# Optimization experiments

Measured on AMD Instinct MI355X. Metric: run time of the kernel, lower is better.

Reference implementation:

```python
import jax, jax.numpy as jnp
import numpy as np

D_MODEL = 768
NHEAD = 12
HEAD_DIM = D_MODEL // NHEAD


def setup_inputs() -> dict:
    key = jax.random.key(0)
    ks = jax.random.split(key, 7)
    s = 1.0 / np.sqrt(D_MODEL)
    x = jax.random.normal(ks[0], (8, 1024, D_MODEL), dtype=jnp.float32)
    Wq = jax.random.uniform(ks[1], (D_MODEL, D_MODEL), jnp.float32, -s, s)
    bq = jax.random.uniform(ks[2], (D_MODEL,), jnp.float32, -s, s)
    Wk = jax.random.uniform(ks[3], (D_MODEL, D_MODEL), jnp.float32, -s, s)
    bk = jax.random.uniform(ks[4], (D_MODEL,), jnp.float32, -s, s)
    Wv = jax.random.uniform(ks[5], (D_MODEL, D_MODEL), jnp.float32, -s, s)
    bv = jax.random.uniform(ks[6], (D_MODEL,), jnp.float32, -s, s)
    return {"x": x, "Wq": Wq, "bq": bq, "Wk": Wk, "bk": bk, "Wv": Wv, "bv": bv}


def reference(x, Wq, bq, Wk, bk, Wv, bv):
    B, S, D = x.shape
    # linear projections (torch Linear: x @ W.T + b)
    q = x @ Wq.T + bq
    k = x @ Wk.T + bk
    v = x @ Wv.T + bv
    # split heads: [B, S, H, Dh] -> [B, H, S, Dh]
    split = lambda t: t.reshape(B, S, NHEAD, HEAD_DIM).transpose(0, 2, 1, 3)
    q, k, v = split(q), split(k), split(v)
    scale = 1.0 / np.sqrt(HEAD_DIM)
    scores = jnp.einsum("bhqd,bhkd->bhqk", q, k) * scale  # [B,H,S,S]
    scores = jax.nn.softmax(scores, axis=-1)  # dropout p=0.0 -> identity
    h = jnp.einsum("bhqk,bhkd->bhqd", scores, v)  # [B,H,S,Dh]
    h = h.transpose(0, 2, 1, 3).reshape(B, S, D)
    return (h, scores)
```

## Files before the change

### kernel.cpp

```cpp
#include <hip/hip_runtime.h>

#define D_MODEL  768
#define NHEAD    12
#define HEAD_DIM 64
#define SEQ      1024
#define BATCH    8
#define NTOK     8192

typedef unsigned short u16;
typedef unsigned int   u32;
typedef float  f32x4  __attribute__((ext_vector_type(4)));
typedef __bf16 bf16x8 __attribute__((ext_vector_type(8)));

#define MFMA(a, b, c) __builtin_amdgcn_mfma_f32_16x16x32_bf16((a), (b), (c), 0, 0, 0)

__device__ __forceinline__ u16 f2bf(float f) {
    u32 u = __float_as_uint(f);
    u += 0x7fffu + ((u >> 16) & 1u);
    return (u16)(u >> 16);
}
__device__ __forceinline__ u32 pack2(float a, float b) {
    return (u32)f2bf(a) | ((u32)f2bf(b) << 16);
}
__device__ __forceinline__ bf16x8 ldfrag(const u16* p) {
    union { uint4 u; bf16x8 b; } c;
    c.u = *(const uint4*)p;
    return c.b;
}
__device__ __forceinline__ bf16x8 u2b(uint4 u) {
    union { uint4 u; bf16x8 b; } c;
    c.u = u;
    return c.b;
}
__device__ __forceinline__ float bflo(u32 u) { return __uint_as_float(u << 16); }
__device__ __forceinline__ float bfhi(u32 u) { return __uint_as_float(u & 0xffff0000u); }

__global__ __launch_bounds__(256)
void qkv_gemm(const float* __restrict__ x,
              const float* __restrict__ Wq, const float* __restrict__ bq,
              const float* __restrict__ Wk, const float* __restrict__ bk,
              const float* __restrict__ Wv, const float* __restrict__ bv,
              u16* __restrict__ qo, u16* __restrict__ ko, u16* __restrict__ vto)
{
    const int m0 = blockIdx.x * 64;
    const int n0 = blockIdx.y * 64;
    const int z  = blockIdx.z;
    const float* W    = (z == 0) ? Wq : (z == 1) ? Wk : Wv;
    const float* bias = (z == 0) ? bq : (z == 1) ? bk : bv;

    __shared__ u16 As[64][72];
    __shared__ u16 Bs[64][72];

    const int t    = threadIdx.x;
    const int lane = t & 63, wave = t >> 6;
    const int grp  = lane >> 4, l16 = lane & 15;
    const int wm   = (wave >> 1) * 32;
    const int wn   = (wave & 1) * 32;
    const int sr   = t >> 2;
    const int sc   = (t & 3) * 16;

    f32x4 acc[2][2] = {};

    for (int kt = 0; kt < D_MODEL; kt += 64) {
        const float* xp = x + (size_t)(m0 + sr) * D_MODEL + kt + sc;
        const float* wp = W + (size_t)(n0 + sr) * D_MODEL + kt + sc;
        const float4 x0 = ((const float4*)xp)[0], x1 = ((const float4*)xp)[1];
        const float4 x2 = ((const float4*)xp)[2], x3 = ((const float4*)xp)[3];
        const float4 w0 = ((const float4*)wp)[0], w1 = ((const float4*)wp)[1];
        const float4 w2 = ((const float4*)wp)[2], w3 = ((const float4*)wp)[3];
        __syncthreads();
        uint4 ua, ub;
        ua.x = pack2(x0.x, x0.y); ua.y = pack2(x0.z, x0.w);
        ua.z = pack2(x1.x, x1.y); ua.w = pack2(x1.z, x1.w);
        ub.x = pack2(x2.x, x2.y); ub.y = pack2(x2.z, x2.w);
        ub.z = pack2(x3.x, x3.y); ub.w = pack2(x3.z, x3.w);
        *(uint4*)&As[sr][sc]     = ua;
        *(uint4*)&As[sr][sc + 8] = ub;
        ua.x = pack2(w0.x, w0.y); ua.y = pack2(w0.z, w0.w);
        ua.z = pack2(w1.x, w1.y); ua.w = pack2(w1.z, w1.w);
        ub.x = pack2(w2.x, w2.y); ub.y = pack2(w2.z, w2.w);
        ub.z = pack2(w3.x, w3.y); ub.w = pack2(w3.z, w3.w);
        *(uint4*)&Bs[sr][sc]     = ua;
        *(uint4*)&Bs[sr][sc + 8] = ub;
        __syncthreads();
#pragma unroll
        for (int ks = 0; ks < 64; ks += 32) {
            const bf16x8 a0 = ldfrag(&As[wm + l16][ks + grp * 8]);
            const bf16x8 a1 = ldfrag(&As[wm + 16 + l16][ks + grp * 8]);
            const bf16x8 b0 = ldfrag(&Bs[wn + l16][ks + grp * 8]);
            const bf16x8 b1 = ldfrag(&Bs[wn + 16 + l16][ks + grp * 8]);
            acc[0][0] = MFMA(a0, b0, acc[0][0]);
            acc[0][1] = MFMA(a0, b1, acc[0][1]);
            acc[1][0] = MFMA(a1, b0, acc[1][0]);
            acc[1][1] = MFMA(a1, b1, acc[1][1]);
        }
    }

    u16* qk_out = (z == 0) ? qo : ko;
#pragma unroll
    for (int tn = 0; tn < 2; ++tn) {
        const int col = n0 + wn + tn * 16 + l16;
        const float bcol = bias[col];
#pragma unroll
        for (int tm = 0; tm < 2; ++tm) {
#pragma unroll
            for (int r = 0; r < 4; ++r) {
                const int row = m0 + wm + tm * 16 + grp * 4 + r;
                const u16 hv = f2bf(acc[tm][tn][r] + bcol);
                if (z < 2) {
                    qk_out[(size_t)row * D_MODEL + col] = hv;
                } else {
                    const int hh = col >> 6, dd = col & 63;
                    const int bb = row >> 10, ss = row & 1023;
                    vto[(((size_t)(bb * NHEAD + hh)) * HEAD_DIM + dd) * SEQ + ss] = hv;
                }
            }
        }
    }
}

__global__ __launch_bounds__(256, 2)
void attn_mfma(const u16* __restrict__ qb, const u16* __restrict__ kb,
               const u16* __restrict__ vtb, float* __restrict__ hout,
               float* __restrict__ sout)
{
    const int qt = blockIdx.x, h = blockIdx.y, b = blockIdx.z;
    const int t    = threadIdx.x;
    const int lane = t & 63, wave = t >> 6;
    const int grp  = lane >> 4, l16 = lane & 15;

    __shared__ u16 Qs[64][72];
    __shared__ u16 Ks[64][72];
    __shared__ u16 Vts[64][72];
    __shared__ u16 Ps[4][16][40];

    const size_t tok0 = (size_t)b * SEQ + qt * 64;
    const int    hb   = h * HEAD_DIM;
    const int    lr   = t >> 3, c0 = (t & 7) * 8;

    {
        const u16* qp = qb + (tok0 + lr) * D_MODEL + hb + c0;
        const uint4 v0 = *(const uint4*)qp;
        const uint4 v1 = *(const uint4*)(qp + (size_t)32 * D_MODEL);
        *(uint4*)&Qs[lr][c0]      = v0;
        *(uint4*)&Qs[lr + 32][c0] = v1;
    }
    __syncthreads();
    const bf16x8 qa0 = ldfrag(&Qs[wave * 16 + l16][grp * 8]);
    const bf16x8 qa1 = ldfrag(&Qs[wave * 16 + l16][32 + grp * 8]);

    const float scale = 0.125f;
    float ssum[4] = {0.f, 0.f, 0.f, 0.f};
    f32x4 accO[4] = {};
    uint4 preg[32];

    const u16* kbase = kb + (size_t)b * SEQ * D_MODEL + hb;
    const u16* vbase = vtb + ((size_t)(b * NHEAD + h) * HEAD_DIM + lr) * SEQ;

#pragma unroll
    for (int kt = 0; kt < 16; ++kt) {
        __syncthreads();
        {
            const u16* kp = kbase + (size_t)(kt * 64 + lr) * D_MODEL + c0;
            const uint4 v0 = *(const uint4*)kp;
            const uint4 v1 = *(const uint4*)(kp + (size_t)32 * D_MODEL);
            const u16* vp = vbase + kt * 64 + c0;
            const uint4 u0 = *(const uint4*)vp;
            const uint4 u1 = *(const uint4*)(vp + (size_t)32 * SEQ);
            *(uint4*)&Ks[lr][c0]       = v0;
            *(uint4*)&Ks[lr + 32][c0]  = v1;
            *(uint4*)&Vts[lr][c0]      = u0;
            *(uint4*)&Vts[lr + 32][c0] = u1;
        }
        __syncthreads();
#pragma unroll
        for (int half = 0; half < 2; ++half) {
#pragma unroll
            for (int sub = 0; sub < 2; ++sub) {
                const int ti = half * 2 + sub;
                const bf16x8 kb0 = ldfrag(&Ks[ti * 16 + l16][grp * 8]);
                const bf16x8 kb1 = ldfrag(&Ks[ti * 16 + l16][32 + grp * 8]);
                f32x4 c = {0.f, 0.f, 0.f, 0.f};
                c = MFMA(qa0, kb0, c);
                c = MFMA(qa1, kb1, c);
#pragma unroll
                for (int r = 0; r < 4; ++r) {
                    const float p = __expf(c[r] * scale);
                    ssum[r] += p;
                    Ps[wave][grp * 4 + r][sub * 16 + l16] = f2bf(p);
                }
            }
            const uint4 pw = *(const uint4*)&Ps[wave][l16][grp * 8];
            preg[kt * 2 + half] = pw;
            const bf16x8 pa = u2b(pw);
#pragma unroll
            for (int c4 = 0; c4 < 4; ++c4) {
                const bf16x8 vb = ldfrag(&Vts[c4 * 16 + l16][half * 32 + grp * 8]);
                accO[c4] = MFMA(pa, vb, accO[c4]);
            }
        }
    }

#pragma unroll
    for (int off = 1; off < 16; off <<= 1)
#pragma unroll
        for (int r = 0; r < 4; ++r) ssum[r] += __shfl_xor(ssum[r], off);
    float sinv[4];
#pragma unroll
    for (int r = 0; r < 4; ++r) sinv[r] = 1.0f / ssum[r];

    const int src = (l16 >> 2) * 16 + l16;
    const float t0 = __shfl(ssum[0], src), t1 = __shfl(ssum[1], src);
    const float t2 = __shfl(ssum[2], src), t3 = __shfl(ssum[3], src);
    const float sa = (l16 & 1) ? t1 : t0;
    const float sb = (l16 & 1) ? t3 : t2;
    const float sinvrow = 1.0f / ((l16 & 2) ? sb : sa);

#pragma unroll
    for (int c4 = 0; c4 < 4; ++c4)
#pragma unroll
        for (int r = 0; r < 4; ++r)
            hout[(tok0 + wave * 16 + grp * 4 + r) * D_MODEL + hb + c4 * 16 + l16] =
                accO[c4][r] * sinv[r];

    float* sp = sout + (size_t)(b * NHEAD + h) * SEQ * SEQ
              + (size_t)(qt * 64 + wave * 16 + l16) * SEQ + grp * 8;
#pragma unroll
    for (int kt = 0; kt < 16; ++kt) {
#pragma unroll
        for (int half = 0; half < 2; ++half) {
            const uint4 pw = preg[kt * 2 + half];
            float4 o0, o1;
            o0.x = bflo(pw.x) * sinvrow; o0.y = bfhi(pw.x) * sinvrow;
            o0.z = bflo(pw.y) * sinvrow; o0.w = bfhi(pw.y) * sinvrow;
            o1.x = bflo(pw.z) * sinvrow; o1.y = bfhi(pw.z) * sinvrow;
            o1.z = bflo(pw.w) * sinvrow; o1.w = bfhi(pw.w) * sinvrow;
            *(float4*)(sp + kt * 64 + half * 32)     = o0;
            *(float4*)(sp + kt * 64 + half * 32 + 4) = o1;
        }
    }
}

extern "C" void kernel_launch(void* const* d_in, const int* in_sizes, int n_in,
                              void* d_out, int out_size, void* d_ws, size_t ws_size,
                              hipStream_t stream)
{
    const float* x  = (const float*)d_in[0];
    const float* Wq = (const float*)d_in[1];
    const float* bq = (const float*)d_in[2];
    const float* Wk = (const float*)d_in[3];
    const float* bk = (const float*)d_in[4];
    const float* Wv = (const float*)d_in[5];
    const float* bv = (const float*)d_in[6];

    float* hout = (float*)d_out;
    float* sout = hout + (size_t)NTOK * D_MODEL;

    u16* qbuf  = (u16*)d_ws;
    u16* kbuf  = qbuf + (size_t)NTOK * D_MODEL;
    u16* vtbuf = kbuf + (size_t)NTOK * D_MODEL;

    qkv_gemm<<<dim3(NTOK / 64, D_MODEL / 64, 3), 256, 0, stream>>>(
        x, Wq, bq, Wk, bk, Wv, bv, qbuf, kbuf, vtbuf);
    attn_mfma<<<dim3(SEQ / 64, NHEAD, BATCH), 256, 0, stream>>>(
        qbuf, kbuf, vtbuf, hout, sout);
}
```

Baseline: 630.3 us.

## Pre-convert inputs to bf16, enlarge GEMM tiles with direct-to-LDS loads, prefetch K/V in attention

Adds a separate kernel that converts x and the three weight matrices to bf16 once, so the QKV GEMM no longer converts fp32 to bf16 inside its loop. The GEMM tile grows from 64x64 to 128x128 with a 4x4 MFMA grid per wave, and operands are loaded with global_load_lds straight into unpadded shared memory. The attention kernel now register-prefetches the next K/V tile while computing the current one. The trade-offs are an extra kernel launch and workspace traffic for the bf16 copies, possible LDS bank conflicts in the unpadded layout, and higher register pressure in attention.

```diff
diff --git a/kernel.cpp b/kernel.cpp
--- a/kernel.cpp
+++ b/kernel.cpp
@@ -35,78 +35,108 @@
 __device__ __forceinline__ float bflo(u32 u) { return __uint_as_float(u << 16); }
 __device__ __forceinline__ float bfhi(u32 u) { return __uint_as_float(u & 0xffff0000u); }
 
+__device__ __forceinline__ void gload16(const u16* g, u16* l) {
+    __builtin_amdgcn_global_load_lds(
+        (const __attribute__((address_space(1))) u32*)(const void*)g,
+        (__attribute__((address_space(3))) u32*)(void*)l, 16, 0, 0);
+}
+__device__ __forceinline__ void bar() {
+    asm volatile("" ::: "memory");
+    __builtin_amdgcn_s_barrier();
+    asm volatile("" ::: "memory");
+}
+
 __global__ __launch_bounds__(256)
-void qkv_gemm(const float* __restrict__ x,
-              const float* __restrict__ Wq, const float* __restrict__ bq,
-              const float* __restrict__ Wk, const float* __restrict__ bk,
-              const float* __restrict__ Wv, const float* __restrict__ bv,
+void cvt_bf16(const float* __restrict__ x,  const float* __restrict__ Wq,
+              const float* __restrict__ Wk, const float* __restrict__ Wv,
+              u16* __restrict__ xb, u16* __restrict__ wb)
+{
+    const size_t NX = (size_t)NTOK * D_MODEL;
+    const size_t NW = (size_t)D_MODEL * D_MODEL;
+    const size_t i  = ((size_t)blockIdx.x * 256 + threadIdx.x) * 8;
+    const float* src; u16* dst; size_t off;
+    if (i < NX) { src = x; dst = xb; off = i; }
+    else {
+        const size_t j = i - NX;
+        const int zz = (int)(j / NW);
+        off = j - (size_t)zz * NW;
+        src = (zz == 0) ? Wq : (zz == 1) ? Wk : Wv;
+        dst = wb + (size_t)zz * NW;
+    }
+    const float4 a = *(const float4*)(src + off);
+    const float4 c = *(const float4*)(src + off + 4);
+    uint4 o;
+    o.x = pack2(a.x, a.y); o.y = pack2(a.z, a.w);
+    o.z = pack2(c.x, c.y); o.w = pack2(c.z, c.w);
+    *(uint4*)(dst + off) = o;
+}
+
+__global__ __launch_bounds__(256)
+void qkv_gemm(const u16* __restrict__ xb, const u16* __restrict__ wb,
+              const float* __restrict__ bq, const float* __restrict__ bk,
+              const float* __restrict__ bv,
               u16* __restrict__ qo, u16* __restrict__ ko, u16* __restrict__ vto)
 {
-    const int m0 = blockIdx.x * 64;
-    const int n0 = blockIdx.y * 64;
+    const int m0 = blockIdx.x * 128;
+    const int n0 = blockIdx.y * 128;
     const int z  = blockIdx.z;
-    const float* W    = (z == 0) ? Wq : (z == 1) ? Wk : Wv;
+    const u16*   W    = wb + (size_t)z * (D_MODEL * D_MODEL);
     const float* bias = (z == 0) ? bq : (z == 1) ? bk : bv;
 
-    __shared__ u16 As[64][72];
-    __shared__ u16 Bs[64][72];
+    __shared__ u16 As[128 * 64];
+    __shared__ u16 Bs[128 * 64];
 
     const int t    = threadIdx.x;
     const int lane = t & 63, wave = t >> 6;
     const int grp  = lane >> 4, l16 = lane & 15;
-    const int wm   = (wave >> 1) * 32;
-    const int wn   = (wave & 1) * 32;
-    const int sr   = t >> 2;
-    const int sc   = (t & 3) * 16;
-
-    f32x4 acc[2][2] = {};
+    const int wm   = (wave >> 1) * 64;
+    const int wn   = (wave & 1) * 64;
+    const int sr   = t >> 3;
+    const int sc   = (t & 7) * 8;
+
+    const u16* ga = xb + (size_t)(m0 + sr) * D_MODEL + sc;
+    const u16* gb = W  + (size_t)(n0 + sr) * D_MODEL + sc;
+    u16* lA = As + wave * 512;
+    u16* lB = Bs + wave * 512;
+
+    f32x4 acc[4][4] = {};
 
     for (int kt = 0; kt < D_MODEL; kt += 64) {
-        const float* xp = x + (size_t)(m0 + sr) * D_MODEL + kt + sc;
-        const float* wp = W + (size_t)(n0 + sr) * D_MODEL + kt + sc;
-        const float4 x0 = ((const float4*)xp)[0], x1 = ((const float4*)xp)[1];
-        const float4 x2 = ((const float4*)xp)[2], x3 = ((const float4*)xp)[3];
-        const float4 w0 = ((const float4*)wp)[0], w1 = ((const float4*)wp)[1];
-        const float4 w2 = ((const float4*)wp)[2], w3 = ((const float4*)wp)[3];
         __syncthreads();
-        uint4 ua, ub;
-        ua.x = pack2(x0.x, x0.y); ua.y = pack2(x0.z, x0.w);
-        ua.z = pack2(x1.x, x1.y); ua.w = pack2(x1.z, x1.w);
-        ub.x = pack2(x2.x, x2.y); ub.y = pack2(x2.z, x2.w);
-        ub.z = pack2(x3.x, x3.y); ub.w = pack2(x3.z, x3.w);
-        *(uint4*)&As[sr][sc]     = ua;
-        *(uint4*)&As[sr][sc + 8] = ub;
-        ua.x = pack2(w0.x, w0.y); ua.y = pack2(w0.z, w0.w);
-        ua.z = pack2(w1.x, w1.y); ua.w = pack2(w1.z, w1.w);
-        ub.x = pack2(w2.x, w2.y); ub.y = pack2(w2.z, w2.w);
-        ub.z = pack2(w3.x, w3.y); ub.w = pack2(w3.z, w3.w);
-        *(uint4*)&Bs[sr][sc]     = ua;
-        *(uint4*)&Bs[sr][sc + 8] = ub;
+#pragma unroll
+        for (int i = 0; i < 4; ++i) {
+            gload16(ga + (size_t)(i * 32) * D_MODEL + kt, lA + i * 2048);
+            gload16(gb + (size_t)(i * 32) * D_MODEL + kt, lB + i * 2048);
+        }
         __syncthreads();
 #pragma unroll
         for (int ks = 0; ks < 64; ks += 32) {
-            const bf16x8 a0 = ldfrag(&As[wm + l16][ks + grp * 8]);
-            const bf16x8 a1 = ldfrag(&As[wm + 16 + l16][ks + grp * 8]);
-            const bf16x8 b0 = ldfrag(&Bs[wn + l16][ks + grp * 8]);
-            const bf16x8 b1 = ldfrag(&Bs[wn + 16 + l16][ks + grp * 8]);
-            acc[0][0] = MFMA(a0, b0, acc[0][0]);
-            acc[0][1] = MFMA(a0, b1, acc[0][1]);
-            acc[1][0] = MFMA(a1, b0, acc[1][0]);
-            acc[1][1] = MFMA(a1, b1, acc[1][1]);
+            bf16x8 af[4], bfr[4];
+#pragma unroll
+            for (int m = 0; m < 4; ++m)
+                af[m] = ldfrag(&As[(wm + m * 16 + l16) * 64 + ks + grp * 8]);
+#pragma unroll
+            for (int n = 0; n < 4; ++n)
+                bfr[n] = ldfrag(&Bs[(wn + n * 16 + l16) * 64 + ks + grp * 8]);
+#pragma unroll
+            for (int m = 0; m < 4; ++m)
+#pragma unroll
+                for (int n = 0; n < 4; ++n)
+                    acc[m][n] = MFMA(af[m], bfr[n], acc[m][n]);
         }
     }
 
     u16* qk_out = (z == 0) ? qo : ko;
 #pragma unroll
-    for (int tn = 0; tn < 2; ++tn) {
-        const int col = n0 + wn + tn * 16 + l16;
+    for (int n = 0; n < 4; ++n) {
+        const int col = n0 + wn + n * 16 + l16;
         const float bcol = bias[col];
 #pragma unroll
-        for (int tm = 0; tm < 2; ++tm) {
+        for (int m = 0; m < 4; ++m) {
 #pragma unroll
             for (int r = 0; r < 4; ++r) {
-                const int row = m0 + wm + tm * 16 + grp * 4 + r;
-                const u16 hv = f2bf(acc[tm][tn][r] + bcol);
+                const int row = m0 + wm + m * 16 + grp * 4 + r;
+                const u16 hv = f2bf(acc[m][n][r] + bcol);
                 if (z < 2) {
                     qk_out[(size_t)row * D_MODEL + col] = hv;
                 } else {
@@ -138,6 +168,19 @@
     const int    hb   = h * HEAD_DIM;
     const int    lr   = t >> 3, c0 = (t & 7) * 8;
 
+    const u16* kbase = kb + (size_t)b * SEQ * D_MODEL + hb;
+    const u16* vbase = vtb + ((size_t)(b * NHEAD + h) * HEAD_DIM + lr) * SEQ;
+
+    uint4 pk0, pk1, pv0, pv1;
+    {
+        const u16* kp = kbase + (size_t)lr * D_MODEL + c0;
+        pk0 = *(const uint4*)kp;
+        pk1 = *(const uint4*)(kp + (size_t)32 * D_MODEL);
+        const u16* vp = vbase + c0;
+        pv0 = *(const uint4*)vp;
+        pv1 = *(const uint4*)(vp + (size_t)32 * SEQ);
+    }
+
     {
         const u16* qp = qb + (tok0 + lr) * D_MODEL + hb + c0;
         const uint4 v0 = *(const uint4*)qp;
@@ -149,30 +192,28 @@
     const bf16x8 qa0 = ldfrag(&Qs[wave * 16 + l16][grp * 8]);
     const bf16x8 qa1 = ldfrag(&Qs[wave * 16 + l16][32 + grp * 8]);
 
+    *(uint4*)&Ks[lr][c0]       = pk0;
+    *(uint4*)&Ks[lr + 32][c0]  = pk1;
+    *(uint4*)&Vts[lr][c0]      = pv0;
+    *(uint4*)&Vts[lr + 32][c0] = pv1;
+    asm volatile("s_waitcnt lgkmcnt(0)" ::: "memory");
+    bar();
+
     const float scale = 0.125f;
     float ssum[4] = {0.f, 0.f, 0.f, 0.f};
     f32x4 accO[4] = {};
     uint4 preg[32];
 
-    const u16* kbase = kb + (size_t)b * SEQ * D_MODEL + hb;
-    const u16* vbase = vtb + ((size_t)(b * NHEAD + h) * HEAD_DIM + lr) * SEQ;
-
 #pragma unroll
     for (int kt = 0; kt < 16; ++kt) {
-        __syncthreads();
-        {
-            const u16* kp = kbase + (size_t)(kt * 64 + lr) * D_MODEL + c0;
-            const uint4 v0 = *(const uint4*)kp;
-            const uint4 v1 = *(const uint4*)(kp + (size_t)32 * D_MODEL);
-            const u16* vp = vbase + kt * 64 + c0;
-            const uint4 u0 = *(const uint4*)vp;
-            const uint4 u1 = *(const uint4*)(vp + (size_t)32 * SEQ);
-            *(uint4*)&Ks[lr][c0]       = v0;
-            *(uint4*)&Ks[lr + 32][c0]  = v1;
-            *(uint4*)&Vts[lr][c0]      = u0;
-            *(uint4*)&Vts[lr + 32][c0] = u1;
-        }
-        __syncthreads();
+        if (kt < 15) {
+            const u16* kp = kbase + (size_t)((kt + 1) * 64 + lr) * D_MODEL + c0;
+            pk0 = *(const uint4*)kp;
+            pk1 = *(const uint4*)(kp + (size_t)32 * D_MODEL);
+            const u16* vp = vbase + (kt + 1) * 64 + c0;
+            pv0 = *(const uint4*)vp;
+            pv1 = *(const uint4*)(vp + (size_t)32 * SEQ);
+        }
 #pragma unroll
         for (int half = 0; half < 2; ++half) {
 #pragma unroll
@@ -198,6 +239,15 @@
                 const bf16x8 vb = ldfrag(&Vts[c4 * 16 + l16][half * 32 + grp * 8]);
                 accO[c4] = MFMA(pa, vb, accO[c4]);
             }
+        }
+        if (kt < 15) {
+            bar();
+            *(uint4*)&Ks[lr][c0]       = pk0;
+            *(uint4*)&Ks[lr + 32][c0]  = pk1;
+            *(uint4*)&Vts[lr][c0]      = pv0;
+            *(uint4*)&Vts[lr + 32][c0] = pv1;
+            asm volatile("s_waitcnt lgkmcnt(0)" ::: "memory");
+            bar();
         }
     }
 
@@ -256,12 +306,18 @@
     float* hout = (float*)d_out;
     float* sout = hout + (size_t)NTOK * D_MODEL;
 
-    u16* qbuf  = (u16*)d_ws;
-    u16* kbuf  = qbuf + (size_t)NTOK * D_MODEL;
-    u16* vtbuf = kbuf + (size_t)NTOK * D_MODEL;
-
-    qkv_gemm<<<dim3(NTOK / 64, D_MODEL / 64, 3), 256, 0, stream>>>(
-        x, Wq, bq, Wk, bk, Wv, bv, qbuf, kbuf, vtbuf);
+    const size_t NX = (size_t)NTOK * D_MODEL;
+    const size_t NW = (size_t)D_MODEL * D_MODEL;
+
+    u16* xb    = (u16*)d_ws;
+    u16* wb    = xb + NX;
+    u16* qbuf  = wb + 3 * NW;
+    u16* kbuf  = qbuf + NX;
+    u16* vtbuf = kbuf + NX;
+
+    cvt_bf16<<<dim3(3936), 256, 0, stream>>>(x, Wq, Wk, Wv, xb, wb);
+    qkv_gemm<<<dim3(NTOK / 128, D_MODEL / 128, 3), 256, 0, stream>>>(
+        xb, wb, bq, bk, bv, qbuf, kbuf, vtbuf);
     attn_mfma<<<dim3(SEQ / 64, NHEAD, BATCH), 256, 0, stream>>>(
         qbuf, kbuf, vtbuf, hout, sout);
 }
```

New measurement: 726.5 us. 1.15x slower.
